# Performance work log

Hardware: AMD Instinct MI355X
Metric: run time of the kernel (lower is better)

The kernel has to match this reference:

```python
import jax, jax.numpy as jnp
import numpy as np
import math

B, S, E = 2, 2048, 2048
H, NOPE, ROPE, V, KVR, DOWN = 16, 64, 32, 64, 256, 2
QKD = NOPE + ROPE
SCALE = QKD ** -0.5
LOW = 4


def setup_inputs() -> dict:
    key = jax.random.key(0)
    ks = jax.random.split(key, 8)
    def w(k, shape):
        return jax.random.normal(k, shape, jnp.float32) * 0.02
    return {
        "hidden_states": jax.random.normal(ks[0], (B, S, E), jnp.float32),
        "wq": w(ks[1], (H * QKD, E)),
        "wkv_a": w(ks[2], (KVR + ROPE, E)),
        "kv_ln_g": jnp.ones((KVR,), jnp.float32),
        "kv_ln_b": jnp.zeros((KVR,), jnp.float32),
        "wkv_b": w(ks[3], (H * (NOPE + V), KVR)),
        "wo": w(ks[4], (E, H * V)),
        "fc_c_w": w(ks[5], (KVR // LOW, KVR)),
        "fc_c_b": jnp.zeros((KVR // LOW,), jnp.float32),
        "fc_p_w": w(ks[6], (KVR // LOW, KVR)),
        "fc_p_b": jnp.zeros((KVR // LOW,), jnp.float32),
    }


def _layernorm(x, g, b, eps=1e-5):
    m = jnp.mean(x, -1, keepdims=True)
    v = jnp.var(x, -1, keepdims=True)
    return (x - m) * jax.lax.rsqrt(v + eps) * g + b


def _pos_enc(T, d):
    # sinusoidal PE: even dims sin, odd dims cos (interleaved)
    pos = jnp.arange(T, dtype=jnp.float32)[:, None]
    div = jnp.exp(jnp.arange(0, d, 2, dtype=jnp.float32) * (-math.log(10000.0) / d))
    ang = pos * div[None, :]
    return jnp.stack([jnp.sin(ang), jnp.cos(ang)], -1).reshape(T, d)


def _rope(x, cos, sin):
    # complex multiply on adjacent pairs, matching torch.view_as_complex path
    xr = x.reshape(x.shape[:-1] + (-1, 2))
    x0, x1 = xr[..., 0], xr[..., 1]
    return jnp.stack([x0 * cos - x1 * sin, x0 * sin + x1 * cos], -1).reshape(x.shape)


def reference(hidden_states, wq, wkv_a, kv_ln_g, kv_ln_b, wkv_b, wo,
              fc_c_w, fc_c_b, fc_p_w, fc_p_b):
    # q projection -> split nope / rope parts
    q = (hidden_states @ wq.T).reshape(B, S, H, QKD)
    q_nope, q_pe = q[..., :NOPE], q[..., NOPE:]
    # low-rank kv projection -> latent + shared rope key
    kv = hidden_states @ wkv_a.T
    kv_c, k_pe = kv[..., :KVR], kv[..., KVR:]
    kv_c = _layernorm(kv_c, kv_ln_g, kv_ln_b)
    # inline partial RoPE (position_ids = arange)
    pos = jnp.arange(S, dtype=jnp.float32)
    freqs = 1.0 / (10000.0 ** (jnp.arange(0, ROPE, 2, dtype=jnp.float32) / ROPE))
    ang = pos[:, None] * freqs[None, :]  # (S, ROPE//2)
    cos, sin = jnp.cos(ang), jnp.sin(ang)
    q_pe = _rope(q_pe, cos[None, :, None, :], sin[None, :, None, :])
    k_pe = _rope(k_pe, cos[None, :, :], sin[None, :, :])
    # hypernetwork gate (train path): C from downsampled PE, repeat_interleave
    t = -(-S // DOWN)
    P = _pos_enc(S, KVR)
    C = jnp.repeat(_pos_enc(t, KVR), DOWN, axis=0)[:S]
    C2 = C @ fc_c_w.T + fc_c_b
    P2 = P @ fc_p_w.T + fc_p_b
    Wg = jax.nn.sigmoid(C2 @ P2.T)  # (S, S)
    r = jnp.arange(S)
    chunk = ((r[:, None] // DOWN) == (r[None, :] // DOWN)) & \
            ((r[:, None] % DOWN) >= (r[None, :] % DOWN))
    Wg = Wg * chunk.astype(Wg.dtype)
    # temporally merged latent KV (simulated compressed cache)
    kv_t = jnp.einsum('ts,bsc->btc', Wg, kv_c)
    k_pe_t = jnp.einsum('ts,bsr->btr', Wg, k_pe)
    # absorbed wkv_b: q_nope into latent space
    wkv_b3 = wkv_b.reshape(H, NOPE + V, KVR)
    q_abs = jnp.einsum('bshd,hdc->bshc', q_nope, wkv_b3[:, :NOPE])
    scores = (jnp.einsum('bshc,btc->bsht', q_abs, kv_t)
              + jnp.einsum('bshr,btr->bsht', q_pe, k_pe_t)) * SCALE
    # stride-aware causal mask: chunk-boundary keys + diagonal
    visible = ((r[None, :] <= r[:, None]) & (((r[None, :] + 1) % DOWN) == 0)) | \
              (r[None, :] == r[:, None])
    mask = jnp.where(visible, 0.0, -1e9).astype(scores.dtype)
    attn = jax.nn.softmax(scores + mask[:, None, :], axis=-1)
    x = jnp.einsum('bsht,btc->bshc', attn, kv_t)
    out = jnp.einsum('bshc,hdc->bshd', x, wkv_b3[:, NOPE:]).reshape(B, S, H * V)
    return out @ wo.T
```

## Files before the change

### kernel.cpp

```cpp
#include <hip/hip_runtime.h>
#include <hip/hip_bf16.h>
#include <math.h>
#include <stdint.h>

#define B_ 2
#define S_ 2048
#define E_ 2048
#define H_ 16
#define NOPE_ 64
#define ROPE_ 32
#define V_ 64
#define KVR_ 256
#define QKD_ 96
#define SCALE_ 0.10206207261596577f

typedef __hip_bfloat16 bf16;
typedef __attribute__((ext_vector_type(8))) short short8;
typedef __attribute__((ext_vector_type(4))) short short4v;
typedef __attribute__((ext_vector_type(4))) float floatx4;

__device__ __forceinline__ float bf2f(bf16 v) { return __bfloat162float(v); }
__device__ __forceinline__ float s2f(short v) {
    bf16 h = *reinterpret_cast<bf16*>(&v);
    return __bfloat162float(h);
}
__device__ __forceinline__ short f2bf_s(float f) {
    bf16 h = __float2bfloat16(f);
    return *reinterpret_cast<short*>(&h);
}
__device__ __forceinline__ void store_c(float* C, size_t i, float v) { C[i] = v; }
__device__ __forceinline__ void store_c(bf16* C, size_t i, float v) { C[i] = __float2bfloat16(v); }

__device__ __forceinline__ void g2l16(const bf16* g, bf16* l) {
    __builtin_amdgcn_global_load_lds(
        (const __attribute__((address_space(1))) void*)g,
        (__attribute__((address_space(3))) void*)l,
        16, 0, 0);
}

__global__ __launch_bounds__(256) void conv_bf16_kernel(const float* __restrict__ src,
                                                        bf16* __restrict__ dst, int n8) {
    int i = blockIdx.x * 256 + threadIdx.x;
    if (i >= n8) return;
    float4 a = ((const float4*)src)[2 * i];
    float4 b = ((const float4*)src)[2 * i + 1];
    short8 r;
    r[0] = f2bf_s(a.x); r[1] = f2bf_s(a.y); r[2] = f2bf_s(a.z); r[3] = f2bf_s(a.w);
    r[4] = f2bf_s(b.x); r[5] = f2bf_s(b.y); r[6] = f2bf_s(b.z); r[7] = f2bf_s(b.w);
    ((short8*)dst)[i] = r;
}

__global__ __launch_bounds__(256) void conv_pad_wkva_kernel(const float* __restrict__ src,
                                                            bf16* __restrict__ dst) {
    int i = blockIdx.x * 256 + threadIdx.x;
    if (i >= 384 * 2048 / 8) return;
    int row = i >> 8;
    short8 r;
    if (row < 288) {
        float4 a = ((const float4*)src)[2 * i];
        float4 b = ((const float4*)src)[2 * i + 1];
        r[0] = f2bf_s(a.x); r[1] = f2bf_s(a.y); r[2] = f2bf_s(a.z); r[3] = f2bf_s(a.w);
        r[4] = f2bf_s(b.x); r[5] = f2bf_s(b.y); r[6] = f2bf_s(b.z); r[7] = f2bf_s(b.w);
    } else {
        for (int j = 0; j < 8; ++j) r[j] = 0;
    }
    ((short8*)dst)[i] = r;
}

__global__ __launch_bounds__(256) void transpose_wkvbT_kernel(const float* __restrict__ wkv_b,
                                                              bf16* __restrict__ wkvbT) {
    int h = blockIdx.x, c = threadIdx.x;
#pragma unroll
    for (int d0 = 0; d0 < 64; d0 += 8) {
        short8 v;
#pragma unroll
        for (int j = 0; j < 8; ++j) v[j] = f2bf_s(wkv_b[(size_t)(h * 128 + d0 + j) * 256 + c]);
        *(short8*)(void*)&wkvbT[((size_t)h * 256 + c) * 64 + d0] = v;
    }
}

template <typename TC>
__global__ __launch_bounds__(256, 2) void gemm_bt_lds(const bf16* __restrict__ A,
                                                      const bf16* __restrict__ Bm,
                                                      TC* __restrict__ C,
                                                      int M, int N, int K) {
    __shared__ bf16 Asf[128 * 32];
    __shared__ bf16 Bsf[128 * 32];
    int tid = threadIdx.x;
    int lane = tid & 63, w = tid >> 6;
    int q4 = lane >> 4, c16 = lane & 15;
    int wr = w >> 1, wc = w & 1;
    int m0 = blockIdx.y * 128, n0 = blockIdx.x * 128;
    floatx4 acc[4][4];
#pragma unroll
    for (int mi = 0; mi < 4; ++mi)
#pragma unroll
        for (int ni = 0; ni < 4; ++ni) acc[mi][ni] = (floatx4){0.f, 0.f, 0.f, 0.f};

    for (int k0 = 0; k0 < K; k0 += 32) {
        __syncthreads();
#pragma unroll
        for (int i = 0; i < 2; ++i) {
            int c = (w << 6) + lane + i * 256;
            int row = c >> 2, kc = c & 3;
            g2l16(&A[(size_t)(m0 + row) * K + k0 + kc * 8], &Asf[c * 8]);
            g2l16(&Bm[(size_t)(n0 + row) * K + k0 + kc * 8], &Bsf[c * 8]);
        }
        __syncthreads();
        short8 af[4], bfr[4];
#pragma unroll
        for (int mi = 0; mi < 4; ++mi)
            af[mi] = *(const short8*)(const void*)&Asf[(wr * 64 + mi * 16 + c16) * 32 + q4 * 8];
#pragma unroll
        for (int ni = 0; ni < 4; ++ni)
            bfr[ni] = *(const short8*)(const void*)&Bsf[(wc * 64 + ni * 16 + c16) * 32 + q4 * 8];
#pragma unroll
        for (int mi = 0; mi < 4; ++mi)
#pragma unroll
            for (int ni = 0; ni < 4; ++ni)
                acc[mi][ni] = __builtin_amdgcn_mfma_f32_16x16x32_bf16(af[mi], bfr[ni], acc[mi][ni], 0, 0, 0);
    }
#pragma unroll
    for (int mi = 0; mi < 4; ++mi)
#pragma unroll
        for (int ni = 0; ni < 4; ++ni)
#pragma unroll
            for (int r = 0; r < 4; ++r) {
                int row = m0 + wr * 64 + mi * 16 + q4 * 4 + r;
                int col = n0 + wc * 64 + ni * 16 + c16;
                store_c(C, (size_t)row * N + col, acc[mi][ni][r]);
            }
}

__global__ __launch_bounds__(256, 2) void gemm_qkv_fused(const bf16* __restrict__ A,
                                                         const bf16* __restrict__ Bq,
                                                         const bf16* __restrict__ Bkv,
                                                         bf16* __restrict__ Cq,
                                                         float* __restrict__ Ckv,
                                                         int K) {
    __shared__ bf16 Asf[128 * 32];
    __shared__ bf16 Bsf[128 * 32];
    int tid = threadIdx.x;
    int lane = tid & 63, w = tid >> 6;
    int q4 = lane >> 4, c16 = lane & 15;
    int wr = w >> 1, wc = w & 1;
    int bx = blockIdx.x;
    bool isq = bx < 12;
    const bf16* Bm = isq ? Bq : Bkv;
    int n0 = isq ? bx * 128 : (bx - 12) * 128;
    int m0 = blockIdx.y * 128;
    floatx4 acc[4][4];
#pragma unroll
    for (int mi = 0; mi < 4; ++mi)
#pragma unroll
        for (int ni = 0; ni < 4; ++ni) acc[mi][ni] = (floatx4){0.f, 0.f, 0.f, 0.f};

    for (int k0 = 0; k0 < K; k0 += 32) {
        __syncthreads();
#pragma unroll
        for (int i = 0; i < 2; ++i) {
            int c = (w << 6) + lane + i * 256;
            int row = c >> 2, kc = c & 3;
            g2l16(&A[(size_t)(m0 + row) * K + k0 + kc * 8], &Asf[c * 8]);
            g2l16(&Bm[(size_t)(n0 + row) * K + k0 + kc * 8], &Bsf[c * 8]);
        }
        __syncthreads();
        short8 af[4], bfr[4];
#pragma unroll
        for (int mi = 0; mi < 4; ++mi)
            af[mi] = *(const short8*)(const void*)&Asf[(wr * 64 + mi * 16 + c16) * 32 + q4 * 8];
#pragma unroll
        for (int ni = 0; ni < 4; ++ni)
            bfr[ni] = *(const short8*)(const void*)&Bsf[(wc * 64 + ni * 16 + c16) * 32 + q4 * 8];
#pragma unroll
        for (int mi = 0; mi < 4; ++mi)
#pragma unroll
            for (int ni = 0; ni < 4; ++ni)
                acc[mi][ni] = __builtin_amdgcn_mfma_f32_16x16x32_bf16(af[mi], bfr[ni], acc[mi][ni], 0, 0, 0);
    }
#pragma unroll
    for (int mi = 0; mi < 4; ++mi)
#pragma unroll
        for (int ni = 0; ni < 4; ++ni)
#pragma unroll
            for (int r = 0; r < 4; ++r) {
                int row = m0 + wr * 64 + mi * 16 + q4 * 4 + r;
                int col = n0 + wc * 64 + ni * 16 + c16;
                if (isq)
                    Cq[(size_t)row * 1536 + col] = __float2bfloat16(acc[mi][ni][r]);
                else
                    Ckv[(size_t)row * 384 + col] = acc[mi][ni][r];
            }
}

template <typename TC>
__global__ __launch_bounds__(256, 4) void gemm64_lds(const bf16* __restrict__ A, int lda, int aoffz,
                                                     const bf16* __restrict__ Bm, int ldb, int boffz,
                                                     TC* __restrict__ C, int ldc, int coffz,
                                                     int K, float scale) {
    int z = blockIdx.z;
    A += (size_t)z * aoffz;
    Bm += (size_t)z * boffz;
    C += (size_t)z * coffz;
    __shared__ bf16 Asf[64 * 32];
    __shared__ bf16 Bsf[64 * 32];
    int tid = threadIdx.x;
    int lane = tid & 63, w = tid >> 6;
    int q4 = lane >> 4, c16 = lane & 15;
    int m0 = blockIdx.y * 64, n0 = blockIdx.x * 64;
    floatx4 acc[4];
#pragma unroll
    for (int ni = 0; ni < 4; ++ni) acc[ni] = (floatx4){0.f, 0.f, 0.f, 0.f};
    int row = tid >> 2, kc = tid & 3;
    for (int k0 = 0; k0 < K; k0 += 32) {
        __syncthreads();
        g2l16(&A[(size_t)(m0 + row) * lda + k0 + kc * 8], &Asf[tid * 8]);
        g2l16(&Bm[(size_t)(n0 + row) * ldb + k0 + kc * 8], &Bsf[tid * 8]);
        __syncthreads();
        short8 af = *(const short8*)(const void*)&Asf[(w * 16 + c16) * 32 + q4 * 8];
#pragma unroll
        for (int ni = 0; ni < 4; ++ni) {
            short8 bfr = *(const short8*)(const void*)&Bsf[(ni * 16 + c16) * 32 + q4 * 8];
            acc[ni] = __builtin_amdgcn_mfma_f32_16x16x32_bf16(af, bfr, acc[ni], 0, 0, 0);
        }
    }
#pragma unroll
    for (int ni = 0; ni < 4; ++ni)
#pragma unroll
        for (int rr = 0; rr < 4; ++rr)
            store_c(C, (size_t)(m0 + w * 16 + q4 * 4 + rr) * ldc + n0 + ni * 16 + c16,
                    acc[ni][rr] * scale);
}

__global__ __launch_bounds__(256) void ln_rope_kernel(const float* __restrict__ kvraw,
                                                      const float* __restrict__ g,
                                                      const float* __restrict__ bta,
                                                      float* __restrict__ kv_c,
                                                      float* __restrict__ kpe) {
    int r = blockIdx.x;
    int tid = threadIdx.x;
    int lane = tid & 63, w = tid >> 6;
    float x = kvraw[(size_t)r * 384 + tid];
    float v1 = x, v2 = x * x;
#pragma unroll
    for (int o = 32; o; o >>= 1) { v1 += __shfl_down(v1, o); v2 += __shfl_down(v2, o); }
    __shared__ float s1[4], s2[4], stats[2];
    if (lane == 0) { s1[w] = v1; s2[w] = v2; }
    __syncthreads();
    if (tid == 0) {
        float S1 = s1[0] + s1[1] + s1[2] + s1[3];
        float S2 = s2[0] + s2[1] + s2[2] + s2[3];
        float mean = S1 / 256.0f;
        float var = S2 / 256.0f - mean * mean;
        stats[0] = mean;
        stats[1] = rsqrtf(var + 1e-5f);
    }
    __syncthreads();
    float y = (x - stats[0]) * stats[1] * g[tid] + bta[tid];
    kv_c[(size_t)r * 256 + tid] = y;
    if (tid < 16) {
        int j = tid;
        int s = r & (S_ - 1);
        float freq = expf(-(float)(2 * j) * 0.28782313662425572f);
        float ang = (float)s * freq;
        float c = cosf(ang), sn = sinf(ang);
        float x0 = kvraw[(size_t)r * 384 + 256 + 2 * j];
        float x1 = kvraw[(size_t)r * 384 + 256 + 2 * j + 1];
        kpe[(size_t)r * 32 + 2 * j]     = x0 * c - x1 * sn;
        kpe[(size_t)r * 32 + 2 * j + 1] = x0 * sn + x1 * c;
    }
}

__global__ __launch_bounds__(64) void c2p2_kernel(const float* __restrict__ fcw_c,
                                                  const float* __restrict__ fcb_c,
                                                  const float* __restrict__ fcw_p,
                                                  const float* __restrict__ fcb_p,
                                                  float* __restrict__ C2,
                                                  float* __restrict__ P2) {
    int t = blockIdx.x;
    int k = threadIdx.x;
    __shared__ float Crow[256], Prow[256];
    for (int i = k; i < 128; i += 64) {
        float div = expf(-(float)i * 0.07195578415606393f);
        float ap = (float)t * div;
        Prow[2 * i]     = sinf(ap);
        Prow[2 * i + 1] = cosf(ap);
        float ac = (float)(t >> 1) * div;
        Crow[2 * i]     = sinf(ac);
        Crow[2 * i + 1] = cosf(ac);
    }
    __syncthreads();
    float sc = fcb_c[k], sp = fcb_p[k];
    for (int c = 0; c < 256; ++c) {
        sc += Crow[c] * fcw_c[(size_t)k * 256 + c];
        sp += Prow[c] * fcw_p[(size_t)k * 256 + c];
    }
    C2[(size_t)t * 64 + k] = sc;
    P2[(size_t)t * 64 + k] = sp;
}

__global__ __launch_bounds__(256) void gates_kernel(const float* __restrict__ C2,
                                                    const float* __restrict__ P2,
                                                    float* __restrict__ g0,
                                                    float* __restrict__ g1) {
    int t = blockIdx.x * 256 + threadIdx.x;
    if (t >= S_) return;
    float d0 = 0.f;
    for (int k = 0; k < 64; ++k) d0 += C2[(size_t)t * 64 + k] * P2[(size_t)t * 64 + k];
    g0[t] = 1.0f / (1.0f + expf(-d0));
    float gg = 0.f;
    if (t & 1) {
        float d1 = 0.f;
        for (int k = 0; k < 64; ++k) d1 += C2[(size_t)t * 64 + k] * P2[(size_t)(t - 1) * 64 + k];
        gg = 1.0f / (1.0f + expf(-d1));
    }
    g1[t] = gg;
}

__global__ __launch_bounds__(256) void kve_kernel(const float* __restrict__ kv_c,
                                                  const float* __restrict__ kpe,
                                                  const float* __restrict__ g0,
                                                  const float* __restrict__ g1,
                                                  bf16* __restrict__ kve_full,
                                                  bf16* __restrict__ kvo) {
    int r = blockIdx.x, tid = threadIdx.x;
    int b = r >> 11, t = r & (S_ - 1);
    float a = g0[t], bb = g1[t];
    float v = a * kv_c[(size_t)r * 256 + tid];
    if (t & 1) v += bb * kv_c[(size_t)(r - 1) * 256 + tid];
    bf16 vb = __float2bfloat16(v);
    kve_full[(size_t)r * 288 + tid] = vb;
    if (t & 1) kvo[((size_t)b * 1024 + (t >> 1)) * 296 + tid] = vb;
    if (tid < 32) {
        float u = a * kpe[(size_t)r * 32 + tid];
        if (t & 1) u += bb * kpe[(size_t)(r - 1) * 32 + tid];
        bf16 ub = __float2bfloat16(u);
        kve_full[(size_t)r * 288 + 256 + tid] = ub;
        if (t & 1) kvo[((size_t)b * 1024 + (t >> 1)) * 296 + 256 + tid] = ub;
    }
}

__global__ __launch_bounds__(256) void kvoT32_kernel(const bf16* __restrict__ kvo,
                                                     bf16* __restrict__ kvoT) {
    int uch = blockIdx.x, b = blockIdx.y;
    int c = threadIdx.x;
    const bf16* src = kvo + ((size_t)b * 1024 + uch * 32) * 296 + c;
    short v[32];
#pragma unroll
    for (int j = 0; j < 32; ++j) v[j] = *(const short*)&src[(size_t)j * 296];
    bf16* dst = kvoT + (((size_t)b * 32 + uch) * 256 + c) * 32;
#pragma unroll
    for (int q = 0; q < 4; ++q) {
        short8 o;
#pragma unroll
        for (int jj = 0; jj < 8; ++jj)
            o[jj] = (jj < 4) ? v[4 * q + jj] : v[16 + 4 * q + (jj - 4)];
        *(short8*)(void*)&dst[q * 8] = o;
    }
}

__global__ __launch_bounds__(256) void rope_qe_kernel(const bf16* __restrict__ q,
                                                      bf16* __restrict__ qe) {
    int idx = blockIdx.x * 256 + threadIdx.x;
    if (idx >= B_ * S_ * H_ * 16) return;
    int j = idx & 15;
    int s = (idx >> 8) & (S_ - 1);
    float freq = expf(-(float)(2 * j) * 0.28782313662425572f);
    float ang = (float)s * freq;
    float c = cosf(ang), sn = sinf(ang);
    size_t row = idx >> 4;
    float a0 = bf2f(q[row * QKD_ + NOPE_ + 2 * j]);
    float a1 = bf2f(q[row * QKD_ + NOPE_ + 2 * j + 1]);
    qe[row * 288 + 256 + 2 * j]     = __float2bfloat16((a0 * c - a1 * sn) * SCALE_);
    qe[row * 288 + 256 + 2 * j + 1] = __float2bfloat16((a0 * sn + a1 * c) * SCALE_);
}

__global__ __launch_bounds__(256) void sscore_kernel(const bf16* __restrict__ qe,
                                                     const bf16* __restrict__ kve_full,
                                                     float* __restrict__ sscore) {
    int s = blockIdx.x, b = blockIdx.y;
    int tid = threadIdx.x;
    int h = tid >> 4, p = tid & 15;
    const bf16* qrow = qe + ((size_t)(b * S_ + s) * H_ + h) * 288;
    const bf16* krow = kve_full + (size_t)(b * S_ + s) * 288;
    float d = 0.f;
#pragma unroll
    for (int e = 0; e < 18; ++e) d += bf2f(qrow[p * 18 + e]) * bf2f(krow[p * 18 + e]);
    d += __shfl_xor(d, 1);
    d += __shfl_xor(d, 2);
    d += __shfl_xor(d, 4);
    d += __shfl_xor(d, 8);
    if (p == 0) sscore[((size_t)(b * S_ + s)) * H_ + h] = d;
}

__global__ __launch_bounds__(256, 3) void attn4_kernel(const bf16* __restrict__ qe,
                                                       const bf16* __restrict__ kvo,
                                                       const bf16* __restrict__ kvoT,
                                                       const bf16* __restrict__ kve_full,
                                                       const float* __restrict__ sscore,
                                                       bf16* __restrict__ xout) {
    int s0 = (int)(gridDim.x - 1 - blockIdx.x) * 4;
    int b = blockIdx.y;
    int tid = threadIdx.x;
    int lane = tid & 63, w = tid >> 6;
    int q4 = lane >> 4, c16 = lane & 15;
    int s = s0 + w;
    int Nodd = (s + 1) >> 1;
    int NoddMax = (s0 + 4) >> 1;
    int niter = (NoddMax + 31) >> 5;

    __shared__ bf16 kvos[32][296];
    __shared__ bf16 kvts[256][32];
    __shared__ bf16 selfr[4][256];

    const bf16* kvob = kvo + (size_t)b * 1024 * 296;
    const bf16* kvoTb = kvoT + (size_t)b * 32 * 8192;

    if (tid < 128) {
        int rr = tid >> 5, ch = tid & 31;
        *(short8*)(void*)&selfr[rr][ch * 8] =
            *(const short8*)(const void*)&kve_full[(size_t)(b * S_ + s0 + rr) * 288 + ch * 8];
    }

    short8 qf[9];
    const bf16* qrow = qe + ((size_t)(b * S_ + s) * H_ + c16) * 288;
#pragma unroll
    for (int kk = 0; kk < 9; ++kk) qf[kk] = *(const short8*)(const void*)&qrow[kk * 32 + q4 * 8];

    floatx4 acc[16];
#pragma unroll
    for (int n = 0; n < 16; ++n) acc[n] = (floatx4){0.f, 0.f, 0.f, 0.f};
    float m_i = -1e30f, l_i = 0.f;

    auto stage = [&](int t) {
        const bf16* sa = kvob + (size_t)t * 32 * 296;
        bf16* la = &kvos[0][0];
#pragma unroll
        for (int i = 0; i < 4; ++i)
            g2l16(&sa[(size_t)(tid + i * 256) * 8], &la[(size_t)(tid + i * 256) * 8]);
        if (tid < 160) g2l16(&sa[(size_t)(tid + 1024) * 8], &la[(size_t)(tid + 1024) * 8]);
        const bf16* sb = kvoTb + (size_t)t * 8192;
        bf16* lb = &kvts[0][0];
#pragma unroll
        for (int i = 0; i < 4; ++i)
            g2l16(&sb[(size_t)(tid + i * 256) * 8], &lb[(size_t)(tid + i * 256) * 8]);
    };

    stage(0);
    __syncthreads();

    for (int it = 0; it < niter; ++it) {
        int u0 = it * 32;
        floatx4 ca0 = (floatx4){0.f, 0.f, 0.f, 0.f}, ca1 = (floatx4){0.f, 0.f, 0.f, 0.f};
        floatx4 cb0 = (floatx4){0.f, 0.f, 0.f, 0.f}, cb1 = (floatx4){0.f, 0.f, 0.f, 0.f};
#pragma unroll
        for (int kk = 0; kk < 9; ++kk) {
            short8 avA = *(const short8*)(const void*)&kvos[c16][kk * 32 + q4 * 8];
            short8 avB = *(const short8*)(const void*)&kvos[16 + c16][kk * 32 + q4 * 8];
            if (kk & 1) {
                ca1 = __builtin_amdgcn_mfma_f32_16x16x32_bf16(avA, qf[kk], ca1, 0, 0, 0);
                cb1 = __builtin_amdgcn_mfma_f32_16x16x32_bf16(avB, qf[kk], cb1, 0, 0, 0);
            } else {
                ca0 = __builtin_amdgcn_mfma_f32_16x16x32_bf16(avA, qf[kk], ca0, 0, 0, 0);
                cb0 = __builtin_amdgcn_mfma_f32_16x16x32_bf16(avB, qf[kk], cb0, 0, 0, 0);
            }
        }
        floatx4 cA = ca0 + ca1;
        floatx4 cB = cb0 + cb1;
        int kA = u0 + q4 * 4;
        int kB = u0 + 16 + q4 * 4;
#pragma unroll
        for (int r = 0; r < 4; ++r) {
            if (kA + r >= Nodd) cA[r] = -1e30f;
            if (kB + r >= Nodd) cB[r] = -1e30f;
        }
        float tmax = fmaxf(fmaxf(fmaxf(cA[0], cA[1]), fmaxf(cA[2], cA[3])),
                           fmaxf(fmaxf(cB[0], cB[1]), fmaxf(cB[2], cB[3])));
        tmax = fmaxf(tmax, __shfl_xor(tmax, 16));
        tmax = fmaxf(tmax, __shfl_xor(tmax, 32));
        float mn = fmaxf(m_i, tmax);
        bool chg = mn > m_i;
        float al = __expf(m_i - mn);
        float pA0 = __expf(cA[0] - mn), pA1 = __expf(cA[1] - mn);
        float pA2 = __expf(cA[2] - mn), pA3 = __expf(cA[3] - mn);
        float pB0 = __expf(cB[0] - mn), pB1 = __expf(cB[1] - mn);
        float pB2 = __expf(cB[2] - mn), pB3 = __expf(cB[3] - mn);
        float rs = (pA0 + pA1 + pA2 + pA3) + (pB0 + pB1 + pB2 + pB3);
        rs += __shfl_xor(rs, 16);
        rs += __shfl_xor(rs, 32);
        l_i = l_i * al + rs;
        m_i = mn;
        if (__any(chg)) {
#pragma unroll
            for (int n = 0; n < 16; ++n) {
                acc[n][0] *= al; acc[n][1] *= al; acc[n][2] *= al; acc[n][3] *= al;
            }
        }
        short8 pf;
        pf[0] = f2bf_s(pA0); pf[1] = f2bf_s(pA1); pf[2] = f2bf_s(pA2); pf[3] = f2bf_s(pA3);
        pf[4] = f2bf_s(pB0); pf[5] = f2bf_s(pB1); pf[6] = f2bf_s(pB2); pf[7] = f2bf_s(pB3);
#pragma unroll
        for (int n = 0; n < 16; ++n) {
            short8 a8 = *(const short8*)(const void*)&kvts[n * 16 + c16][q4 * 8];
            acc[n] = __builtin_amdgcn_mfma_f32_16x16x32_bf16(a8, pf, acc[n], 0, 0, 0);
        }
        __syncthreads();
        if (it + 1 < niter) stage(it + 1);
        __syncthreads();
    }

    if ((s & 1) == 0) {
        float scs = sscore[((size_t)(b * S_ + s)) * H_ + c16];
        float mn = fmaxf(m_i, scs);
        float al = __expf(m_i - mn);
        float pp = __expf(scs - mn);
        l_i = l_i * al + pp;
        m_i = mn;
#pragma unroll
        for (int n = 0; n < 16; ++n) {
            short4v kv4 = *(const short4v*)(const void*)&selfr[w][n * 16 + q4 * 4];
#pragma unroll
            for (int r = 0; r < 4; ++r)
                acc[n][r] = acc[n][r] * al + pp * s2f(kv4[r]);
        }
    }

    float invl = 1.0f / l_i;
    bf16* orow = xout + ((size_t)(b * S_ + s) * H_ + c16) * 256;
#pragma unroll
    for (int n = 0; n < 16; ++n) {
        short4v o;
        o[0] = f2bf_s(acc[n][0] * invl);
        o[1] = f2bf_s(acc[n][1] * invl);
        o[2] = f2bf_s(acc[n][2] * invl);
        o[3] = f2bf_s(acc[n][3] * invl);
        *(short4v*)(void*)&orow[n * 16 + q4 * 4] = o;
    }
}

extern "C" void kernel_launch(void* const* d_in, const int* in_sizes, int n_in,
                              void* d_out, int out_size, void* d_ws, size_t ws_size,
                              hipStream_t stream) {
    const float* hs     = (const float*)d_in[0];
    const float* wq     = (const float*)d_in[1];
    const float* wkv_a  = (const float*)d_in[2];
    const float* ln_g   = (const float*)d_in[3];
    const float* ln_b   = (const float*)d_in[4];
    const float* wkv_b  = (const float*)d_in[5];
    const float* wo     = (const float*)d_in[6];
    const float* fc_c_w = (const float*)d_in[7];
    const float* fc_c_b = (const float*)d_in[8];
    const float* fc_p_w = (const float*)d_in[9];
    const float* fc_p_b = (const float*)d_in[10];
    float* out = (float*)d_out;
    (void)in_sizes; (void)n_in; (void)out_size; (void)ws_size;

    const int M = B_ * S_;
    char* wsb = (char*)d_ws;
    size_t o = 0;
    auto alloc = [&](size_t bytes) { char* p = wsb + o; o += (bytes + 255) & ~(size_t)255; return p; };

    bf16* qe = (bf16*)alloc((size_t)M * H_ * 288 * 2);
    char* region2 = alloc((size_t)M * H_ * 256 * 2);
    bf16* hs_bf    = (bf16*)region2;
    bf16* wq_bf    = (bf16*)(region2 + (size_t)M * E_ * 2);
    bf16* wkva_pad = (bf16*)(region2 + (size_t)M * E_ * 2 + (size_t)1536 * E_ * 2);
    bf16* x_bf     = (bf16*)region2;
    char* region3 = alloc((size_t)M * 1536 * 2);
    bf16* q_bf    = (bf16*)region3;
    bf16* outp_bf = (bf16*)region3;
    float* kvraw = (float*)alloc((size_t)M * 384 * 4);
    float* kv_c  = (float*)alloc((size_t)M * 256 * 4);
    float* kpe   = (float*)alloc((size_t)M * 32 * 4);
    bf16* wo_bf   = (bf16*)alloc((size_t)E_ * 1024 * 2);
    bf16* wkvb_bf = (bf16*)alloc((size_t)2048 * 256 * 2);
    bf16* wkvbT   = (bf16*)alloc((size_t)H_ * 256 * 64 * 2);
    bf16* kve_full = (bf16*)alloc((size_t)M * 288 * 2);
    bf16* kvo      = (bf16*)alloc((size_t)B_ * 1024 * 296 * 2);
    bf16* kvoT     = (bf16*)alloc((size_t)B_ * 32 * 8192 * 2);
    float* sscore  = (float*)alloc((size_t)M * H_ * 4);
    float* C2 = (float*)alloc((size_t)S_ * 64 * 4);
    float* P2 = (float*)alloc((size_t)S_ * 64 * 4);
    float* g0 = (float*)alloc(S_ * 4);
    float* g1 = (float*)alloc(S_ * 4);

    conv_bf16_kernel<<<(M * E_ / 8 + 255) / 256, 256, 0, stream>>>(hs, hs_bf, M * E_ / 8);
    conv_bf16_kernel<<<(1536 * E_ / 8 + 255) / 256, 256, 0, stream>>>(wq, wq_bf, 1536 * E_ / 8);
    conv_bf16_kernel<<<(E_ * 1024 / 8 + 255) / 256, 256, 0, stream>>>(wo, wo_bf, E_ * 1024 / 8);
    conv_bf16_kernel<<<(2048 * 256 / 8 + 255) / 256, 256, 0, stream>>>(wkv_b, wkvb_bf, 2048 * 256 / 8);
    conv_pad_wkva_kernel<<<(384 * 2048 / 8 + 255) / 256, 256, 0, stream>>>(wkv_a, wkva_pad);
    transpose_wkvbT_kernel<<<H_, 256, 0, stream>>>(wkv_b, wkvbT);
    gemm_qkv_fused<<<dim3(15, M / 128), 256, 0, stream>>>(hs_bf, wq_bf, wkva_pad, q_bf, kvraw, E_);
    ln_rope_kernel<<<M, 256, 0, stream>>>(kvraw, ln_g, ln_b, kv_c, kpe);
    c2p2_kernel<<<S_, 64, 0, stream>>>(fc_c_w, fc_c_b, fc_p_w, fc_p_b, C2, P2);
    gates_kernel<<<(S_ + 255) / 256, 256, 0, stream>>>(C2, P2, g0, g1);
    kve_kernel<<<M, 256, 0, stream>>>(kv_c, kpe, g0, g1, kve_full, kvo);
    kvoT32_kernel<<<dim3(32, B_), 256, 0, stream>>>(kvo, kvoT);
    gemm64_lds<bf16><<<dim3(256 / 64, M / 64, H_), 256, 0, stream>>>(
        q_bf, H_ * QKD_, QKD_, wkvbT, 64, 256 * 64, qe, H_ * 288, 288, 64, SCALE_);
    rope_qe_kernel<<<(M * H_ * 16 + 255) / 256, 256, 0, stream>>>(q_bf, qe);
    sscore_kernel<<<dim3(S_, B_), 256, 0, stream>>>(qe, kve_full, sscore);
    attn4_kernel<<<dim3(S_ / 4, B_), 256, 0, stream>>>(qe, kvo, kvoT, kve_full, sscore, x_bf);
    gemm64_lds<bf16><<<dim3(1, M / 64, H_), 256, 0, stream>>>(
        x_bf, H_ * 256, 256, wkvb_bf + (size_t)64 * 256, 256, 128 * 256, outp_bf, 1024, 64, 256, 1.0f);
    gemm_bt_lds<float><<<dim3(E_ / 128, M / 128), 256, 0, stream>>>(outp_bf, wo_bf, out, M, E_, 1024);
}
```

Baseline: 363.5 us.

## Double-buffer attention KV tiles and fuse fp32-to-bf16 conversion launches

The attention kernel now keeps two LDS buffers for the KV tiles. It issues the global-to-LDS load for the next tile before computing on the current one, which removes one barrier per iteration and lets loads overlap the MFMA work. MFMA sections are wrapped in s_setprio raises. Launch bounds drop from 3 to 2 blocks per CU because LDS use roughly doubles. The five separate fp32-to-bf16 conversion launches are merged into one kernel that branches on index range, saving launch overhead.

```diff
diff --git a/kernel.cpp b/kernel.cpp
--- a/kernel.cpp
+++ b/kernel.cpp
@@ -38,33 +38,50 @@
         16, 0, 0);
 }
 
-__global__ __launch_bounds__(256) void conv_bf16_kernel(const float* __restrict__ src,
-                                                        bf16* __restrict__ dst, int n8) {
+#define CV_N0 1048576
+#define CV_N1 (CV_N0 + 393216)
+#define CV_N2 (CV_N1 + 262144)
+#define CV_N3 (CV_N2 + 65536)
+#define CV_N4 (CV_N3 + 98304)
+__global__ __launch_bounds__(256) void conv_fused_kernel(const float* __restrict__ hs,
+                                                         const float* __restrict__ wq,
+                                                         const float* __restrict__ wo,
+                                                         const float* __restrict__ wkv_b,
+                                                         const float* __restrict__ wkv_a,
+                                                         bf16* __restrict__ hs_bf,
+                                                         bf16* __restrict__ wq_bf,
+                                                         bf16* __restrict__ wo_bf,
+                                                         bf16* __restrict__ wkvb_bf,
+                                                         bf16* __restrict__ wkva_pad) {
     int i = blockIdx.x * 256 + threadIdx.x;
-    if (i >= n8) return;
-    float4 a = ((const float4*)src)[2 * i];
-    float4 b = ((const float4*)src)[2 * i + 1];
+    const float* src;
+    bf16* dst;
+    int j;
+    if (i < CV_N0)      { src = hs;    dst = hs_bf;   j = i; }
+    else if (i < CV_N1) { src = wq;    dst = wq_bf;   j = i - CV_N0; }
+    else if (i < CV_N2) { src = wo;    dst = wo_bf;   j = i - CV_N1; }
+    else if (i < CV_N3) { src = wkv_b; dst = wkvb_bf; j = i - CV_N2; }
+    else if (i < CV_N4) {
+        j = i - CV_N3;
+        int row = j >> 8;
+        short8 r;
+        if (row < 288) {
+            float4 a = ((const float4*)wkv_a)[2 * j];
+            float4 b = ((const float4*)wkv_a)[2 * j + 1];
+            r[0] = f2bf_s(a.x); r[1] = f2bf_s(a.y); r[2] = f2bf_s(a.z); r[3] = f2bf_s(a.w);
+            r[4] = f2bf_s(b.x); r[5] = f2bf_s(b.y); r[6] = f2bf_s(b.z); r[7] = f2bf_s(b.w);
+        } else {
+            for (int k = 0; k < 8; ++k) r[k] = 0;
+        }
+        ((short8*)wkva_pad)[j] = r;
+        return;
+    } else return;
+    float4 a = ((const float4*)src)[2 * j];
+    float4 b = ((const float4*)src)[2 * j + 1];
     short8 r;
     r[0] = f2bf_s(a.x); r[1] = f2bf_s(a.y); r[2] = f2bf_s(a.z); r[3] = f2bf_s(a.w);
     r[4] = f2bf_s(b.x); r[5] = f2bf_s(b.y); r[6] = f2bf_s(b.z); r[7] = f2bf_s(b.w);
-    ((short8*)dst)[i] = r;
-}
-
-__global__ __launch_bounds__(256) void conv_pad_wkva_kernel(const float* __restrict__ src,
-                                                            bf16* __restrict__ dst) {
-    int i = blockIdx.x * 256 + threadIdx.x;
-    if (i >= 384 * 2048 / 8) return;
-    int row = i >> 8;
-    short8 r;
-    if (row < 288) {
-        float4 a = ((const float4*)src)[2 * i];
-        float4 b = ((const float4*)src)[2 * i + 1];
-        r[0] = f2bf_s(a.x); r[1] = f2bf_s(a.y); r[2] = f2bf_s(a.z); r[3] = f2bf_s(a.w);
-        r[4] = f2bf_s(b.x); r[5] = f2bf_s(b.y); r[6] = f2bf_s(b.z); r[7] = f2bf_s(b.w);
-    } else {
-        for (int j = 0; j < 8; ++j) r[j] = 0;
-    }
-    ((short8*)dst)[i] = r;
+    ((short8*)dst)[j] = r;
 }
 
 __global__ __launch_bounds__(256) void transpose_wkvbT_kernel(const float* __restrict__ wkv_b,
@@ -393,7 +410,7 @@
     if (p == 0) sscore[((size_t)(b * S_ + s)) * H_ + h] = d;
 }
 
-__global__ __launch_bounds__(256, 3) void attn4_kernel(const bf16* __restrict__ qe,
+__global__ __launch_bounds__(256, 2) void attn5_kernel(const bf16* __restrict__ qe,
                                                        const bf16* __restrict__ kvo,
                                                        const bf16* __restrict__ kvoT,
                                                        const bf16* __restrict__ kve_full,
@@ -409,8 +426,8 @@
     int NoddMax = (s0 + 4) >> 1;
     int niter = (NoddMax + 31) >> 5;
 
-    __shared__ bf16 kvos[32][296];
-    __shared__ bf16 kvts[256][32];
+    __shared__ bf16 kvos[2][32][296];
+    __shared__ bf16 kvts[2][256][32];
     __shared__ bf16 selfr[4][256];
 
     const bf16* kvob = kvo + (size_t)b * 1024 * 296;
@@ -432,31 +449,35 @@
     for (int n = 0; n < 16; ++n) acc[n] = (floatx4){0.f, 0.f, 0.f, 0.f};
     float m_i = -1e30f, l_i = 0.f;
 
-    auto stage = [&](int t) {
+    auto stage = [&](int t, int p) {
         const bf16* sa = kvob + (size_t)t * 32 * 296;
-        bf16* la = &kvos[0][0];
+        bf16* la = &kvos[p][0][0];
 #pragma unroll
         for (int i = 0; i < 4; ++i)
             g2l16(&sa[(size_t)(tid + i * 256) * 8], &la[(size_t)(tid + i * 256) * 8]);
         if (tid < 160) g2l16(&sa[(size_t)(tid + 1024) * 8], &la[(size_t)(tid + 1024) * 8]);
         const bf16* sb = kvoTb + (size_t)t * 8192;
-        bf16* lb = &kvts[0][0];
+        bf16* lb = &kvts[p][0][0];
 #pragma unroll
         for (int i = 0; i < 4; ++i)
             g2l16(&sb[(size_t)(tid + i * 256) * 8], &lb[(size_t)(tid + i * 256) * 8]);
     };
 
-    stage(0);
+    stage(0, 0);
     __syncthreads();
 
     for (int it = 0; it < niter; ++it) {
+        int p = it & 1;
+        if (it + 1 < niter) stage(it + 1, 1 - p);
+
         int u0 = it * 32;
         floatx4 ca0 = (floatx4){0.f, 0.f, 0.f, 0.f}, ca1 = (floatx4){0.f, 0.f, 0.f, 0.f};
         floatx4 cb0 = (floatx4){0.f, 0.f, 0.f, 0.f}, cb1 = (floatx4){0.f, 0.f, 0.f, 0.f};
+        __builtin_amdgcn_s_setprio(1);
 #pragma unroll
         for (int kk = 0; kk < 9; ++kk) {
-            short8 avA = *(const short8*)(const void*)&kvos[c16][kk * 32 + q4 * 8];
-            short8 avB = *(const short8*)(const void*)&kvos[16 + c16][kk * 32 + q4 * 8];
+            short8 avA = *(const short8*)(const void*)&kvos[p][c16][kk * 32 + q4 * 8];
+            short8 avB = *(const short8*)(const void*)&kvos[p][16 + c16][kk * 32 + q4 * 8];
             if (kk & 1) {
                 ca1 = __builtin_amdgcn_mfma_f32_16x16x32_bf16(avA, qf[kk], ca1, 0, 0, 0);
                 cb1 = __builtin_amdgcn_mfma_f32_16x16x32_bf16(avB, qf[kk], cb1, 0, 0, 0);
@@ -465,6 +486,7 @@
                 cb0 = __builtin_amdgcn_mfma_f32_16x16x32_bf16(avB, qf[kk], cb0, 0, 0, 0);
             }
         }
+        __builtin_amdgcn_s_setprio(0);
         floatx4 cA = ca0 + ca1;
         floatx4 cB = cb0 + cb1;
         int kA = u0 + q4 * 4;
@@ -499,13 +521,13 @@
         short8 pf;
         pf[0] = f2bf_s(pA0); pf[1] = f2bf_s(pA1); pf[2] = f2bf_s(pA2); pf[3] = f2bf_s(pA3);
         pf[4] = f2bf_s(pB0); pf[5] = f2bf_s(pB1); pf[6] = f2bf_s(pB2); pf[7] = f2bf_s(pB3);
+        __builtin_amdgcn_s_setprio(1);
 #pragma unroll
         for (int n = 0; n < 16; ++n) {
-            short8 a8 = *(const short8*)(const void*)&kvts[n * 16 + c16][q4 * 8];
+            short8 a8 = *(const short8*)(const void*)&kvts[p][n * 16 + c16][q4 * 8];
             acc[n] = __builtin_amdgcn_mfma_f32_16x16x32_bf16(a8, pf, acc[n], 0, 0, 0);
         }
-        __syncthreads();
-        if (it + 1 < niter) stage(it + 1);
+        __builtin_amdgcn_s_setprio(0);
         __syncthreads();
     }
 
@@ -584,11 +606,8 @@
     float* g0 = (float*)alloc(S_ * 4);
     float* g1 = (float*)alloc(S_ * 4);
 
-    conv_bf16_kernel<<<(M * E_ / 8 + 255) / 256, 256, 0, stream>>>(hs, hs_bf, M * E_ / 8);
-    conv_bf16_kernel<<<(1536 * E_ / 8 + 255) / 256, 256, 0, stream>>>(wq, wq_bf, 1536 * E_ / 8);
-    conv_bf16_kernel<<<(E_ * 1024 / 8 + 255) / 256, 256, 0, stream>>>(wo, wo_bf, E_ * 1024 / 8);
-    conv_bf16_kernel<<<(2048 * 256 / 8 + 255) / 256, 256, 0, stream>>>(wkv_b, wkvb_bf, 2048 * 256 / 8);
-    conv_pad_wkva_kernel<<<(384 * 2048 / 8 + 255) / 256, 256, 0, stream>>>(wkv_a, wkva_pad);
+    conv_fused_kernel<<<(CV_N4 + 255) / 256, 256, 0, stream>>>(
+        hs, wq, wo, wkv_b, wkv_a, hs_bf, wq_bf, wo_bf, wkvb_bf, wkva_pad);
     transpose_wkvbT_kernel<<<H_, 256, 0, stream>>>(wkv_b, wkvbT);
     gemm_qkv_fused<<<dim3(15, M / 128), 256, 0, stream>>>(hs_bf, wq_bf, wkva_pad, q_bf, kvraw, E_);
     ln_rope_kernel<<<M, 256, 0, stream>>>(kvraw, ln_g, ln_b, kv_c, kpe);
@@ -600,7 +619,7 @@
         q_bf, H_ * QKD_, QKD_, wkvbT, 64, 256 * 64, qe, H_ * 288, 288, 64, SCALE_);
     rope_qe_kernel<<<(M * H_ * 16 + 255) / 256, 256, 0, stream>>>(q_bf, qe);
     sscore_kernel<<<dim3(S_, B_), 256, 0, stream>>>(qe, kve_full, sscore);
-    attn4_kernel<<<dim3(S_ / 4, B_), 256, 0, stream>>>(qe, kvo, kvoT, kve_full, sscore, x_bf);
+    attn5_kernel<<<dim3(S_ / 4, B_), 256, 0, stream>>>(qe, kvo, kvoT, kve_full, sscore, x_bf);
     gemm64_lds<bf16><<<dim3(1, M / 64, H_), 256, 0, stream>>>(
         x_bf, H_ * 256, 256, wkvb_bf + (size_t)64 * 256, 256, 128 * 256, outp_bf, 1024, 64, 256, 1.0f);
     gemm_bt_lds<float><<<dim3(E_ / 128, M / 128), 256, 0, stream>>>(outp_bf, wo_bf, out, M, E_, 1024);
```

New measurement: 355.2 us. 1.02x faster.
